# Performance work log

Measured on AMD Instinct MI355X. Metric: run time of the kernel, lower is better.

Reference implementation:

```python
import jax, jax.numpy as jnp
import numpy as np

NEG_SLOPE = 0.2
EPS = 1e-16  # PyG softmax denominator epsilon


def gat_conv(x, edge_index, W, a_src, a_dst, bias):
    """PyG GATConv, heads=1, concat=True, add_self_loops=True, edge_dim=None."""
    N = x.shape[0]
    h = x @ W  # [N, d]
    loops = jnp.arange(N)
    src = jnp.concatenate([edge_index[0], loops])  # [E+N]
    dst = jnp.concatenate([edge_index[1], loops])
    # per-node attention dot-products, gathered per edge
    s = h @ a_src  # [N]
    t = h @ a_dst  # [N]
    e = jax.nn.leaky_relu(s[src] + t[dst], NEG_SLOPE)  # [E+N]
    # segment softmax over incoming edges of each dst node
    m = jax.ops.segment_max(e, dst, num_segments=N)
    ex = jnp.exp(e - m[dst])
    denom = jax.ops.segment_sum(ex, dst, num_segments=N)
    alpha = ex / (denom[dst] + EPS)  # [E+N]
    out = jax.ops.segment_sum(h[src] * alpha[:, None], dst, num_segments=N)
    return out + bias


def setup_inputs() -> dict:
    key = jax.random.key(0)
    N, E, D, DE = 50000, 600000, 128, 16
    ks = jax.random.split(key, 12)
    scale = 1.0 / np.sqrt(D)
    return {
        "x_one": jax.random.normal(ks[0], (N, D), jnp.float32),
        "edge_index_one": jax.random.randint(ks[1], (2, E), 0, N, jnp.int64),
        "edge_attr_emb_one": jax.random.normal(ks[2], (E, DE), jnp.float32),
        "x_two": jax.random.normal(ks[3], (N, D), jnp.float32),
        "edge_index_two": jax.random.randint(ks[4], (2, E), 0, N, jnp.int64),
        "edge_attr_emb_two": jax.random.normal(ks[5], (E, DE), jnp.float32),
        "W1": jax.random.normal(ks[6], (D, D), jnp.float32) * scale,
        "a_src1": jax.random.normal(ks[7], (D,), jnp.float32) * scale,
        "a_dst1": jax.random.normal(ks[8], (D,), jnp.float32) * scale,
        "b1": jnp.zeros((D,), jnp.float32),
        "W2": jax.random.normal(ks[9], (D, D), jnp.float32) * scale,
        "a_src2": jax.random.normal(ks[10], (D,), jnp.float32) * scale,
        "a_dst2": jax.random.normal(ks[11], (D,), jnp.float32) * scale,
        "b2": jnp.zeros((D,), jnp.float32),
    }


def reference(x_one, edge_index_one, edge_attr_emb_one,
              x_two, edge_index_two, edge_attr_emb_two,
              W1, a_src1, a_dst1, b1, W2, a_src2, a_dst2, b2):
    # edge_attr is ignored: GATConv was built without edge_dim.
    # F.dropout(training=False) is identity in eval mode.
    out_one = jax.nn.relu(gat_conv(x_one, edge_index_one, W1, a_src1, a_dst1, b1))
    out_two = jax.nn.relu(gat_conv(x_two, edge_index_two, W2, a_src2, a_dst2, b2))
    return (out_one, out_two)
```

## Files before the change

kernel.cpp:

```cpp
#include <hip/hip_runtime.h>
#include <math.h>

#define D 128
#define NEG_SLOPE 0.2f
#define EPS 1e-16f
#define PT 4096
#define SCAP 1024
#define SLOTS 64
#define SSTR 66

typedef __attribute__((ext_vector_type(8))) __bf16 bf16x8;
typedef __attribute__((ext_vector_type(4))) float f32x4;
typedef __attribute__((ext_vector_type(2))) float f32x2;

__device__ __forceinline__ unsigned short f2bf(float f) {
    return __builtin_bit_cast(unsigned short, (__bf16)f);
}
__device__ __forceinline__ unsigned long long pack4bf(float a, float b, float c, float d) {
    return (unsigned long long)f2bf(a)
         | ((unsigned long long)f2bf(b) << 16)
         | ((unsigned long long)f2bf(c) << 32)
         | ((unsigned long long)f2bf(d) << 48);
}
__device__ __forceinline__ f32x2 bf2f2(unsigned u) {
    f32x2 r;
    r.x = __uint_as_float(u << 16);
    r.y = __uint_as_float(u & 0xffff0000u);
    return r;
}

__global__ __launch_bounds__(256) void k_gemm(const float* __restrict__ X0,
                                              const float* __restrict__ X1,
                                              const float* __restrict__ W0,
                                              const float* __restrict__ W1,
                                              const float* __restrict__ as0,
                                              const float* __restrict__ as1,
                                              const float* __restrict__ ad0,
                                              const float* __restrict__ ad1,
                                              unsigned short* __restrict__ Hb,
                                              float* __restrict__ sv,
                                              float* __restrict__ tv,
                                              int* __restrict__ fill,
                                              int N, int nb, int NSB) {
    __shared__ char lds[32768];
    const int t = threadIdx.x;
    {
        int gi = blockIdx.x * 256 + t;
        if (gi < NSB) fill[gi] = gi * SCAP;
    }
    const int g = (blockIdx.x >= nb) ? 1 : 0;
    const int row0 = (blockIdx.x - g * nb) * 128;
    const float* X = g ? X1 : X0;
    const float* W = g ? W1 : W0;
    const float* a_src = g ? as1 : as0;
    const float* a_dst = g ? ad1 : ad0;
    const int gbase = g * N;

    {
        const int n = t & 127;
        const int khalf = (t >> 7) * 64;
        #pragma unroll 4
        for (int i = 0; i < 16; ++i) {
            const int k0 = khalf + i * 4;
            float f0 = W[(size_t)(k0 + 0) * D + n];
            float f1 = W[(size_t)(k0 + 1) * D + n];
            float f2 = W[(size_t)(k0 + 2) * D + n];
            float f3 = W[(size_t)(k0 + 3) * D + n];
            int off = (n * 256 + k0 * 2) ^ ((n & 7) << 4);
            *(unsigned long long*)(lds + off) = pack4bf(f0, f1, f2, f3);
        }
    }
    __syncthreads();

    const int w = t >> 6;
    const int l = t & 63;
    const int lr = l & 15;
    const int lg = l >> 4;
    const int m0 = row0 + w * 32 + lr;
    const int m1 = m0 + 16;
    const float4* X4 = (const float4*)X;

    f32x4 acc[2][8];
    #pragma unroll
    for (int r = 0; r < 2; ++r)
        #pragma unroll
        for (int nt = 0; nt < 8; ++nt) acc[r][nt] = (f32x4){0.f, 0.f, 0.f, 0.f};

    #pragma unroll
    for (int kk = 0; kk < 4; ++kk) {
        const int kByte = kk * 64 + lg * 16;
        float4 xa0 = make_float4(0.f, 0.f, 0.f, 0.f), xa1 = xa0, xb0 = xa0, xb1 = xa0;
        const int fidx = kk * 8 + lg * 2;
        if (m0 < N) {
            xa0 = X4[(size_t)m0 * 32 + fidx];
            xa1 = X4[(size_t)m0 * 32 + fidx + 1];
        }
        if (m1 < N) {
            xb0 = X4[(size_t)m1 * 32 + fidx];
            xb1 = X4[(size_t)m1 * 32 + fidx + 1];
        }
        ulonglong2 ua, ub;
        ua.x = pack4bf(xa0.x, xa0.y, xa0.z, xa0.w);
        ua.y = pack4bf(xa1.x, xa1.y, xa1.z, xa1.w);
        ub.x = pack4bf(xb0.x, xb0.y, xb0.z, xb0.w);
        ub.y = pack4bf(xb1.x, xb1.y, xb1.z, xb1.w);
        bf16x8 a0 = __builtin_bit_cast(bf16x8, ua);
        bf16x8 a1 = __builtin_bit_cast(bf16x8, ub);
        #pragma unroll
        for (int nt = 0; nt < 8; ++nt) {
            const int n = nt * 16 + lr;
            bf16x8 b = *(const bf16x8*)(lds + ((n * 256 + kByte) ^ ((n & 7) << 4)));
            acc[0][nt] = __builtin_amdgcn_mfma_f32_16x16x32_bf16(a0, b, acc[0][nt], 0, 0, 0);
            acc[1][nt] = __builtin_amdgcn_mfma_f32_16x16x32_bf16(a1, b, acc[1][nt], 0, 0, 0);
        }
    }

    float asv[8], adv[8];
    #pragma unroll
    for (int nt = 0; nt < 8; ++nt) {
        asv[nt] = a_src[nt * 16 + lr];
        adv[nt] = a_dst[nt * 16 + lr];
    }
    #pragma unroll
    for (int r = 0; r < 2; ++r) {
        #pragma unroll
        for (int reg = 0; reg < 4; ++reg) {
            const int row = row0 + w * 32 + r * 16 + lg * 4 + reg;
            float ss = 0.f, tt = 0.f;
            #pragma unroll
            for (int nt = 0; nt < 8; ++nt) {
                float hv = acc[r][nt][reg];
                ss += hv * asv[nt];
                tt += hv * adv[nt];
                if (row < N) Hb[(size_t)(gbase + row) * D + nt * 16 + lr] = f2bf(hv);
            }
            #pragma unroll
            for (int off = 8; off; off >>= 1) {
                ss += __shfl_xor(ss, off);
                tt += __shfl_xor(tt, off);
            }
            if (lr == 0 && row < N) { sv[gbase + row] = ss; tv[gbase + row] = tt; }
        }
    }
}

__global__ __launch_bounds__(256) void k_part(const int* __restrict__ s0,
                                              const int* __restrict__ d0,
                                              const int* __restrict__ s1,
                                              const int* __restrict__ d1,
                                              int* __restrict__ fill,
                                              unsigned* __restrict__ P,
                                              int E0, int Et, int N, int NSB) {
    __shared__ int hcnt[2048];
    __shared__ int hbase[2048];
    const int t = threadIdx.x;
    const int i0 = blockIdx.x * PT;
    const int i1 = min(i0 + PT, Et);
    for (int i = t; i < NSB; i += 256) hcnt[i] = 0;
    __syncthreads();
    for (int i = i0 + t; i < i1; i += 256) {
        int dd = (i < E0) ? d0[i] : d1[i - E0] + N;
        atomicAdd(&hcnt[dd >> 6], 1);
    }
    __syncthreads();
    for (int i = t; i < NSB; i += 256) {
        int c = hcnt[i];
        hbase[i] = c ? atomicAdd(&fill[i], c) : 0;
        hcnt[i] = 0;
    }
    __syncthreads();
    for (int i = i0 + t; i < i1; i += 256) {
        int ss, dd;
        if (i < E0) { ss = s0[i]; dd = d0[i]; }
        else        { ss = s1[i - E0] + N; dd = d1[i - E0] + N; }
        int sb = dd >> 6;
        int pos = hbase[sb] + atomicAdd(&hcnt[sb], 1);
        if (pos < (sb + 1) * SCAP)
            P[pos] = (unsigned)ss | ((unsigned)(dd & 63) << 26);
    }
}

__global__ __launch_bounds__(256) void k_gatherf(const unsigned* __restrict__ P,
                                                 const int* __restrict__ fill,
                                                 const float* __restrict__ sv,
                                                 const float* __restrict__ tv,
                                                 const unsigned short* __restrict__ Hb,
                                                 const float* __restrict__ b0,
                                                 const float* __restrict__ b1,
                                                 float* __restrict__ out, int N, int M) {
    __shared__ uint2 ep[32 * SSTR];
    __shared__ int cnt[32];
    __shared__ float dsum[32];
    __shared__ float tvl[32];
    const int t = threadIdx.x;
    const int pb = blockIdx.x >> 1;
    const int half = blockIdx.x & 1;
    const int dbase = blockIdx.x << 5;
    const int bstart = pb * SCAP;
    int bend = fill[pb];
    if (bend > bstart + SCAP) bend = bstart + SCAP;

    if (t < 32) {
        int d = dbase + t;
        int dc = min(d, M - 1);
        float tvd = tv[dc];
        tvl[t] = tvd;
        float es = sv[dc] + tvd;
        es = (es > 0.f) ? es : NEG_SLOPE * es;
        float ps = __expf(es);
        bool ok = (d < M);
        ep[t * SSTR] = make_uint2((unsigned)dc, ok ? __float_as_uint(ps) : 0u);
        cnt[t] = 1;
        dsum[t] = ok ? ps : 1.f;
    }
    __syncthreads();
    for (int i = bstart + t; i < bend; i += 256) {
        unsigned w = P[i];
        int dl6 = (int)(w >> 26);
        if ((dl6 >> 5) == half) {
            int dlo = dl6 & 31;
            int src = (int)(w & 0x03FFFFFFu);
            float e = sv[src] + tvl[dlo];
            e = (e > 0.f) ? e : NEG_SLOPE * e;
            float p = __expf(e);
            int pos = atomicAdd(&cnt[dlo], 1);
            if (pos < SLOTS) ep[dlo * SSTR + pos] = make_uint2((unsigned)src, __float_as_uint(p));
            atomicAdd(&dsum[dlo], p);
        }
    }
    __syncthreads();
    if (t < 32) {
        int c = min(cnt[t], SLOTS);
        int c4 = min((c + 3) & ~3, SLOTS);
        unsigned dsrc = (unsigned)min(dbase + t, M - 1);
        for (int k = c; k < c4; ++k) ep[t * SSTR + k] = make_uint2(dsrc, 0u);
        cnt[t] = c4;
    }
    __syncthreads();

    const int wv = t >> 6;
    const int lane = t & 63;
    const int qtr = lane >> 4;
    const int sl = lane & 15;
    const int qid = wv * 4 + qtr;

    #pragma unroll
    for (int r = 0; r < 2; ++r) {
        const int ld = qid + r * 16;
        const int d = dbase + ld;
        const int dg = cnt[ld];
        const int base = ld * SSTR;

        f32x2 a0 = {0.f, 0.f}, a1 = {0.f, 0.f}, a2 = {0.f, 0.f}, a3 = {0.f, 0.f};
        for (int j = 0; j < dg; j += 4) {
            uint2 e0 = ep[base + j];
            uint2 e1 = ep[base + j + 1];
            uint2 e2 = ep[base + j + 2];
            uint2 e3 = ep[base + j + 3];
            float p0 = __uint_as_float(e0.y);
            float p1 = __uint_as_float(e1.y);
            float p2 = __uint_as_float(e2.y);
            float p3 = __uint_as_float(e3.y);
            uint4 w0 = *(const uint4*)(Hb + (size_t)e0.x * D + sl * 8);
            uint4 w1 = *(const uint4*)(Hb + (size_t)e1.x * D + sl * 8);
            uint4 w2 = *(const uint4*)(Hb + (size_t)e2.x * D + sl * 8);
            uint4 w3 = *(const uint4*)(Hb + (size_t)e3.x * D + sl * 8);
            a0 += p0 * bf2f2(w0.x); a1 += p0 * bf2f2(w0.y); a2 += p0 * bf2f2(w0.z); a3 += p0 * bf2f2(w0.w);
            a0 += p1 * bf2f2(w1.x); a1 += p1 * bf2f2(w1.y); a2 += p1 * bf2f2(w1.z); a3 += p1 * bf2f2(w1.w);
            a0 += p2 * bf2f2(w2.x); a1 += p2 * bf2f2(w2.y); a2 += p2 * bf2f2(w2.z); a3 += p2 * bf2f2(w2.w);
            a0 += p3 * bf2f2(w3.x); a1 += p3 * bf2f2(w3.y); a2 += p3 * bf2f2(w3.z); a3 += p3 * bf2f2(w3.w);
        }

        if (d < M) {
            const float* bp = ((d < N) ? b0 : b1) + sl * 8;
            float inv = 1.0f / (dsum[ld] + EPS);
            float4 o0, o1;
            o0.x = fmaxf(a0.x * inv + bp[0], 0.f);
            o0.y = fmaxf(a0.y * inv + bp[1], 0.f);
            o0.z = fmaxf(a1.x * inv + bp[2], 0.f);
            o0.w = fmaxf(a1.y * inv + bp[3], 0.f);
            o1.x = fmaxf(a2.x * inv + bp[4], 0.f);
            o1.y = fmaxf(a2.y * inv + bp[5], 0.f);
            o1.z = fmaxf(a3.x * inv + bp[6], 0.f);
            o1.w = fmaxf(a3.y * inv + bp[7], 0.f);
            float4* op = (float4*)(out + (size_t)d * D + sl * 8);
            op[0] = o0;
            op[1] = o1;
        }
    }
}

static inline size_t rup(size_t x) { return (x + 255) & ~(size_t)255; }

extern "C" void kernel_launch(void* const* d_in, const int* in_sizes, int n_in,
                              void* d_out, int out_size, void* d_ws, size_t ws_size,
                              hipStream_t stream) {
    const int N = in_sizes[0] / D;
    const int M = 2 * N;
    const int E0 = in_sizes[1] / 2;
    const int E1 = in_sizes[4] / 2;
    const int Et = E0 + E1;
    const int NSB = (M + 63) >> 6;
    const int NGB = (M + 31) >> 5;
    float* out = (float*)d_out;

    char* ws = (char*)d_ws;
    unsigned short* Hb = (unsigned short*)ws; ws += rup((size_t)M * D * sizeof(unsigned short));
    float* sv = (float*)ws;       ws += rup((size_t)M * sizeof(float));
    float* tv = (float*)ws;       ws += rup((size_t)M * sizeof(float));
    int* fill = (int*)ws;         ws += rup((size_t)NSB * sizeof(int));
    unsigned* P = (unsigned*)ws;

    const int* EI0 = (const int*)d_in[1];
    const int* EI1 = (const int*)d_in[4];
    const int* s0 = EI0, *d0 = EI0 + E0;
    const int* s1 = EI1, *d1 = EI1 + E1;

    const int nb = (N + 127) / 128;

    k_gemm<<<2 * nb, 256, 0, stream>>>((const float*)d_in[0], (const float*)d_in[3],
                                       (const float*)d_in[6], (const float*)d_in[10],
                                       (const float*)d_in[7], (const float*)d_in[11],
                                       (const float*)d_in[8], (const float*)d_in[12],
                                       Hb, sv, tv, fill, N, nb, NSB);
    k_part<<<(Et + PT - 1) / PT, 256, 0, stream>>>(s0, d0, s1, d1, fill, P, E0, Et, N, NSB);
    k_gatherf<<<NGB, 256, 0, stream>>>(P, fill, sv, tv, Hb,
                                       (const float*)d_in[9], (const float*)d_in[13],
                                       out, N, M);
}
```

Measured before the change: 104.3 us.

## Fuse edge partitioning into GEMM launch as extra blocks, zero counters via memset

The edge partition kernel is merged into the GEMM kernel as additional blocks, so partitioning runs alongside the projection GEMM instead of after it. Bucket fill counters now start at zero and are cleared by a hipMemsetAsync, with the bucket base offset added at use time. This removes a launch boundary and lets the atomic-heavy partition work overlap the compute-bound GEMM. In exchange it adds a memset launch, and the two block types now compete for LDS and CUs within one grid.

```diff
diff --git a/kernel.cpp b/kernel.cpp
--- a/kernel.cpp
+++ b/kernel.cpp
@@ -29,25 +29,59 @@
     return r;
 }
 
-__global__ __launch_bounds__(256) void k_gemm(const float* __restrict__ X0,
-                                              const float* __restrict__ X1,
-                                              const float* __restrict__ W0,
-                                              const float* __restrict__ W1,
-                                              const float* __restrict__ as0,
-                                              const float* __restrict__ as1,
-                                              const float* __restrict__ ad0,
-                                              const float* __restrict__ ad1,
-                                              unsigned short* __restrict__ Hb,
-                                              float* __restrict__ sv,
-                                              float* __restrict__ tv,
-                                              int* __restrict__ fill,
-                                              int N, int nb, int NSB) {
+__global__ __launch_bounds__(256) void k_fused(const float* __restrict__ X0,
+                                               const float* __restrict__ X1,
+                                               const float* __restrict__ W0,
+                                               const float* __restrict__ W1,
+                                               const float* __restrict__ as0,
+                                               const float* __restrict__ as1,
+                                               const float* __restrict__ ad0,
+                                               const float* __restrict__ ad1,
+                                               unsigned short* __restrict__ Hb,
+                                               float* __restrict__ sv,
+                                               float* __restrict__ tv,
+                                               const int* __restrict__ s0,
+                                               const int* __restrict__ d0,
+                                               const int* __restrict__ s1,
+                                               const int* __restrict__ d1,
+                                               int* __restrict__ ucnt,
+                                               unsigned* __restrict__ P,
+                                               int N, int nb, int nb2,
+                                               int E0, int Et, int NSB) {
     __shared__ char lds[32768];
     const int t = threadIdx.x;
-    {
-        int gi = blockIdx.x * 256 + t;
-        if (gi < NSB) fill[gi] = gi * SCAP;
-    }
+
+    if (blockIdx.x >= nb2) {
+        int* hcnt = (int*)lds;
+        int* hbase = (int*)(lds + 8192);
+        const int bid = blockIdx.x - nb2;
+        const int i0 = bid * PT;
+        const int i1 = min(i0 + PT, Et);
+        for (int i = t; i < NSB; i += 256) hcnt[i] = 0;
+        __syncthreads();
+        for (int i = i0 + t; i < i1; i += 256) {
+            int dd = (i < E0) ? d0[i] : d1[i - E0] + N;
+            atomicAdd(&hcnt[dd >> 6], 1);
+        }
+        __syncthreads();
+        for (int i = t; i < NSB; i += 256) {
+            int c = hcnt[i];
+            hbase[i] = c ? (i * SCAP + atomicAdd(&ucnt[i], c)) : 0;
+            hcnt[i] = 0;
+        }
+        __syncthreads();
+        for (int i = i0 + t; i < i1; i += 256) {
+            int ss, dd;
+            if (i < E0) { ss = s0[i]; dd = d0[i]; }
+            else        { ss = s1[i - E0] + N; dd = d1[i - E0] + N; }
+            int sb = dd >> 6;
+            int pos = hbase[sb] + atomicAdd(&hcnt[sb], 1);
+            if (pos < (sb + 1) * SCAP)
+                P[pos] = (unsigned)ss | ((unsigned)(dd & 63) << 26);
+        }
+        return;
+    }
+
     const int g = (blockIdx.x >= nb) ? 1 : 0;
     const int row0 = (blockIdx.x - g * nb) * 128;
     const float* X = g ? X1 : X0;
@@ -144,44 +178,8 @@
     }
 }
 
-__global__ __launch_bounds__(256) void k_part(const int* __restrict__ s0,
-                                              const int* __restrict__ d0,
-                                              const int* __restrict__ s1,
-                                              const int* __restrict__ d1,
-                                              int* __restrict__ fill,
-                                              unsigned* __restrict__ P,
-                                              int E0, int Et, int N, int NSB) {
-    __shared__ int hcnt[2048];
-    __shared__ int hbase[2048];
-    const int t = threadIdx.x;
-    const int i0 = blockIdx.x * PT;
-    const int i1 = min(i0 + PT, Et);
-    for (int i = t; i < NSB; i += 256) hcnt[i] = 0;
-    __syncthreads();
-    for (int i = i0 + t; i < i1; i += 256) {
-        int dd = (i < E0) ? d0[i] : d1[i - E0] + N;
-        atomicAdd(&hcnt[dd >> 6], 1);
-    }
-    __syncthreads();
-    for (int i = t; i < NSB; i += 256) {
-        int c = hcnt[i];
-        hbase[i] = c ? atomicAdd(&fill[i], c) : 0;
-        hcnt[i] = 0;
-    }
-    __syncthreads();
-    for (int i = i0 + t; i < i1; i += 256) {
-        int ss, dd;
-        if (i < E0) { ss = s0[i]; dd = d0[i]; }
-        else        { ss = s1[i - E0] + N; dd = d1[i - E0] + N; }
-        int sb = dd >> 6;
-        int pos = hbase[sb] + atomicAdd(&hcnt[sb], 1);
-        if (pos < (sb + 1) * SCAP)
-            P[pos] = (unsigned)ss | ((unsigned)(dd & 63) << 26);
-    }
-}
-
 __global__ __launch_bounds__(256) void k_gatherf(const unsigned* __restrict__ P,
-                                                 const int* __restrict__ fill,
+                                                 const int* __restrict__ ucnt,
                                                  const float* __restrict__ sv,
                                                  const float* __restrict__ tv,
                                                  const unsigned short* __restrict__ Hb,
@@ -197,8 +195,7 @@
     const int half = blockIdx.x & 1;
     const int dbase = blockIdx.x << 5;
     const int bstart = pb * SCAP;
-    int bend = fill[pb];
-    if (bend > bstart + SCAP) bend = bstart + SCAP;
+    const int bend = bstart + min(ucnt[pb], SCAP);
 
     if (t < 32) {
         int d = dbase + t;
@@ -302,13 +299,14 @@
     const int Et = E0 + E1;
     const int NSB = (M + 63) >> 6;
     const int NGB = (M + 31) >> 5;
+    const int NPART = (Et + PT - 1) / PT;
     float* out = (float*)d_out;
 
     char* ws = (char*)d_ws;
     unsigned short* Hb = (unsigned short*)ws; ws += rup((size_t)M * D * sizeof(unsigned short));
     float* sv = (float*)ws;       ws += rup((size_t)M * sizeof(float));
     float* tv = (float*)ws;       ws += rup((size_t)M * sizeof(float));
-    int* fill = (int*)ws;         ws += rup((size_t)NSB * sizeof(int));
+    int* ucnt = (int*)ws;         ws += rup((size_t)NSB * sizeof(int));
     unsigned* P = (unsigned*)ws;
 
     const int* EI0 = (const int*)d_in[1];
@@ -317,14 +315,17 @@
     const int* s1 = EI1, *d1 = EI1 + E1;
 
     const int nb = (N + 127) / 128;
-
-    k_gemm<<<2 * nb, 256, 0, stream>>>((const float*)d_in[0], (const float*)d_in[3],
-                                       (const float*)d_in[6], (const float*)d_in[10],
-                                       (const float*)d_in[7], (const float*)d_in[11],
-                                       (const float*)d_in[8], (const float*)d_in[12],
-                                       Hb, sv, tv, fill, N, nb, NSB);
-    k_part<<<(Et + PT - 1) / PT, 256, 0, stream>>>(s0, d0, s1, d1, fill, P, E0, Et, N, NSB);
-    k_gatherf<<<NGB, 256, 0, stream>>>(P, fill, sv, tv, Hb,
+    const int nb2 = 2 * nb;
+
+    hipMemsetAsync(ucnt, 0, (size_t)NSB * sizeof(int), stream);
+
+    k_fused<<<nb2 + NPART, 256, 0, stream>>>(
+        (const float*)d_in[0], (const float*)d_in[3],
+        (const float*)d_in[6], (const float*)d_in[10],
+        (const float*)d_in[7], (const float*)d_in[11],
+        (const float*)d_in[8], (const float*)d_in[12],
+        Hb, sv, tv, s0, d0, s1, d1, ucnt, P, N, nb, nb2, E0, Et, NSB);
+    k_gatherf<<<NGB, 256, 0, stream>>>(P, ucnt, sv, tv, Hb,
                                        (const float*)d_in[9], (const float*)d_in[13],
                                        out, N, M);
 }
```

Result: faster. 99.95 us (-4.1%).
